# Optimization experiments

Measured on AMD Instinct MI355X. Metric: run time of the kernel, lower is better.

## Reference

```python
import jax, jax.numpy as jnp
import numpy as np

S, B, C = 56, 32, 1024
T = 48
H = 1024          # hidden_size_decoder (== context_size C)
EMB = 512
RANK = 128
VOCAB = 32000


def setup_inputs() -> dict:
    key = jax.random.key(0)
    ks = jax.random.split(key, 16)
    w = 0.05
    inp = {
        "encoded": jax.random.normal(ks[0], (S, B, C), jnp.float32),
        "encoder_state": jax.random.normal(ks[1], (2, B, H), jnp.float32) * 0.1,
        "tgt_tokens": jax.random.randint(ks[2], (B, T), 0, VOCAB),
        "enc_lens": jax.random.randint(ks[3], (B,), S // 2, S + 1).astype(jnp.int32),
        "tgt_lens": jax.random.randint(ks[4], (B,), T // 2, T + 1).astype(jnp.int32),
        "E": jax.random.normal(ks[5], (VOCAB, RANK), jnp.float32) * w,
        "P": jax.random.normal(ks[6], (RANK, EMB), jnp.float32) * w,
        "W0": jax.random.normal(ks[7], (EMB + C, 4 * H), jnp.float32) * w,
        "U0": jax.random.normal(ks[8], (H, 4 * H), jnp.float32) * w,
        "b0": jnp.zeros((4 * H,), jnp.float32),
        "W1": jax.random.normal(ks[9], (H, 4 * H), jnp.float32) * w,
        "U1": jax.random.normal(ks[10], (H, 4 * H), jnp.float32) * w,
        "b1": jnp.zeros((4 * H,), jnp.float32),
        "Wo": jax.random.normal(ks[11], (H + C, EMB), jnp.float32) * w,
        "bo": jnp.zeros((EMB,), jnp.float32),
    }
    return inp


def _lstm_cell(x, h, c, W, U, b):
    gates = x @ W + h @ U + b                      # [B, 4H]
    i, f, g, o = jnp.split(gates, 4, axis=-1)      # torch LSTMCell gate order
    c_new = jax.nn.sigmoid(f) * c + jax.nn.sigmoid(i) * jnp.tanh(g)
    h_new = jax.nn.sigmoid(o) * jnp.tanh(c_new)
    return h_new, c_new


def reference(encoded, encoder_state, tgt_tokens, enc_lens, tgt_lens,
              E, P, W0, U0, b0, W1, U1, b1, Wo, bo):
    # encoded: [S, B, C] (padded encoder outputs), encoder_state: [L=2, B, H]
    enc_b = jnp.transpose(encoded, (1, 0, 2))                 # [B, S, C]
    enc_mask = jnp.arange(S)[None, :] >= enc_lens[:, None]    # [B, S] True = pad

    # factorized embedding lookup (dropout p=0)
    emb = (E[tgt_tokens] @ P)                                 # [B, T, EMB]
    emb_t = jnp.transpose(emb, (1, 0, 2))[: T - 1]            # [T-1, B, EMB]

    h0 = encoder_state                                        # [2, B, H]
    c0 = jnp.zeros_like(encoder_state)
    ctx0 = jnp.zeros((B, C), encoded.dtype)

    def step(carry, x_emb):
        h, c, ctx = carry
        x = jnp.concatenate([x_emb, ctx], axis=-1)            # [B, EMB+C]
        h0n, c0n = _lstm_cell(x, h[0], c[0], W0, U0, b0)
        h1n, c1n = _lstm_cell(h0n, h[1], c[1], W1, U1, b1)
        query = h1n                                           # no context projection
        scores = jnp.einsum("bsc,bc->bs", enc_b, query)       # [B, S]
        scores = jnp.where(enc_mask, -jnp.inf, scores)
        p_att = jax.nn.softmax(scores, axis=-1)
        ctx_new = jnp.einsum("bs,bsc->bc", p_att, enc_b)      # [B, C]
        return (jnp.stack([h0n, h1n]), jnp.stack([c0n, c1n]), ctx_new), (h1n, ctx_new)

    _, (decs, ctxs) = jax.lax.scan(step, (h0, c0, ctx0), emb_t)  # each [T-1, B, *]

    feats = jnp.concatenate([decs, ctxs], axis=-1)            # [T-1, B, H+C]
    hproj = jnp.tanh(feats @ Wo + bo)                          # [T-1, B, EMB]
    logits = (hproj @ P.T) @ E.T                               # [T-1, B, VOCAB]

    labels = tgt_tokens[:, 1:].T                               # [T-1, B]
    logp = jax.nn.log_softmax(logits, axis=-1)
    nll = -jnp.take_along_axis(logp, labels[..., None], axis=-1)[..., 0]
    valid = jnp.arange(T - 1)[:, None] < (tgt_lens[None, :] - 1)  # step t predicts token t+1
    loss = jnp.sum(jnp.where(valid, nll, 0.0))                 # CrossEntropyLoss(reduction='sum')
    return loss
```

## Files before the change

kernel.cpp:

```cpp
#include <hip/hip_runtime.h>
#include <math.h>

#define S_   56
#define B_   32
#define C_   1024
#define T_   48
#define TS   47
#define H_   1024
#define EMB_ 512
#define RANK_ 128
#define VOCAB_ 32000
#define G4   4096
#define NBLK 256

#define FL_DONE 8192
#define FL_P    8224
#define FL_PD   9248
#define FL_SIZE 10240

using bf16x8 = __attribute__((ext_vector_type(8))) __bf16;
using f32x4  = __attribute__((ext_vector_type(4))) float;

__device__ __forceinline__ float sigmoidf_(float x){ return 1.0f/(1.0f+expf(-x)); }
__device__ __forceinline__ float b2f(__bf16 x){ return (float)x; }
__device__ __forceinline__ f32x4 z4(){ f32x4 z = {0.f,0.f,0.f,0.f}; return z; }

#define AG __HIP_MEMORY_SCOPE_AGENT
__device__ __forceinline__ void stc_u64(void* p, unsigned long long v){
  __hip_atomic_store((unsigned long long*)p, v, __ATOMIC_RELAXED, AG);
}
__device__ __forceinline__ void stc_bf16(__bf16* p, __bf16 v){
  union { __bf16 b; unsigned short s; } t; t.b = v;
  __hip_atomic_store((unsigned short*)p, t.s, __ATOMIC_RELAXED, AG);
}

struct RedShared {
  float red[4][2][16][18];
};
struct AttnShared {
  union { float hS[1024]; float cred[3][128][8]; } u;
  float sS[64];
  float pS[64];
};
union alignas(16) SharedU { RedShared r; AttnShared a; };

__device__ __forceinline__ void bar_arrive(unsigned* bars, int bi, unsigned e){
  asm volatile("s_waitcnt vmcnt(0)" ::: "memory");
  __syncthreads();
  if (threadIdx.x == 0)
    __hip_atomic_store(bars + (size_t)bi*32, e, __ATOMIC_RELAXED, AG);
}
__device__ __forceinline__ void bar_wait(unsigned* bars, int bi, unsigned e){
  if (bi == 0){
    if (threadIdx.x < 256){
      while (__hip_atomic_load(bars + (size_t)threadIdx.x*32, __ATOMIC_RELAXED, AG) < e)
        __builtin_amdgcn_s_sleep(1);
    }
    __syncthreads();
    if (threadIdx.x == 0)
      __hip_atomic_store(bars + FL_DONE, e, __ATOMIC_RELAXED, AG);
  } else {
    if (threadIdx.x == 0){
      while (__hip_atomic_load(bars + FL_DONE, __ATOMIC_RELAXED, AG) < e)
        __builtin_amdgcn_s_sleep(1);
    }
    __syncthreads();
  }
  asm volatile("" ::: "memory");
}
__device__ __forceinline__ void pflag_wait(unsigned* bars, int bi, unsigned t){
  if (bi == 0){
    if (threadIdx.x < 32){
      while (__hip_atomic_load(bars + FL_P + (size_t)threadIdx.x*32, __ATOMIC_RELAXED, AG) < t)
        __builtin_amdgcn_s_sleep(1);
    }
    __syncthreads();
    if (threadIdx.x == 0)
      __hip_atomic_store(bars + FL_PD, t, __ATOMIC_RELAXED, AG);
  } else {
    if (threadIdx.x == 0){
      while (__hip_atomic_load(bars + FL_PD, __ATOMIC_RELAXED, AG) < t)
        __builtin_amdgcn_s_sleep(1);
    }
    __syncthreads();
  }
  asm volatile("" ::: "memory");
}

__global__ void k_init(const float* __restrict__ es, __bf16* h0bm1, __bf16* fm1,
                       unsigned* bars){
  int i = blockIdx.x*blockDim.x + threadIdx.x;
  if (i < 32*H_){
    int b = i >> 10, j = i & 1023;
    h0bm1[(size_t)b*1024 + j]       = (__bf16)es[i];
    fm1[(size_t)b*2048 + j]         = (__bf16)es[32*H_ + i];
    fm1[(size_t)b*2048 + 1024 + j]  = (__bf16)0.0f;
  }
  if (i < FL_SIZE) bars[i] = 0u;
}

__global__ void k_cvt(const float* __restrict__ src, __bf16* __restrict__ dst, int n){
  int i = (blockIdx.x*blockDim.x + threadIdx.x)*4;
  if (i < n){
    float4 v = *(const float4*)(src + i);
    dst[i+0]=(__bf16)v.x; dst[i+1]=(__bf16)v.y; dst[i+2]=(__bf16)v.z; dst[i+3]=(__bf16)v.w;
  }
}

__global__ void k_embed(const float* __restrict__ E, const float* __restrict__ P,
                        const int* __restrict__ tok, __bf16* __restrict__ embb){
  int blk = blockIdx.x;
  int t = blk >> 5, b = blk & 31, tid = threadIdx.x;
  __shared__ float er[RANK_];
  int tk = tok[b*T_ + t];
  er[tid] = E[(size_t)tk*RANK_ + tid];
  __syncthreads();
  float4 acc = {0.f,0.f,0.f,0.f};
  int e = tid*4;
  for (int r2 = 0; r2 < RANK_; r2++){
    float ev = er[r2];
    float4 p = *(const float4*)(P + (size_t)r2*EMB_ + e);
    acc.x += ev*p.x; acc.y += ev*p.y; acc.z += ev*p.z; acc.w += ev*p.w;
  }
  size_t o = (size_t)blk*EMB_ + e;
  embb[o+0]=(__bf16)acc.x; embb[o+1]=(__bf16)acc.y;
  embb[o+2]=(__bf16)acc.z; embb[o+3]=(__bf16)acc.w;
}

__global__ void k_pack2(const float* __restrict__ W, int K1, const float* __restrict__ U,
                        __bf16* __restrict__ dst, int NCH){
  int ch = blockIdx.x;
  int g  = blockIdx.y >> 2;
  int band = blockIdx.y & 3;
  int tid = threadIdx.x;
  __shared__ __bf16 Tl[32][264];
  {
    int r = tid>>3, cs = tid&7;
    int kk = ch*32 + r;
    const float* src = (kk < K1) ? (W + (size_t)kk*G4 + g*1024 + band*256 + cs*32)
                                 : (U + (size_t)(kk-K1)*G4 + g*1024 + band*256 + cs*32);
    #pragma unroll
    for (int u=0;u<8;u++){
      float4 v = *(const float4*)(src + u*4);
      Tl[r][cs*32+u*4+0]=(__bf16)v.x; Tl[r][cs*32+u*4+1]=(__bf16)v.y;
      Tl[r][cs*32+u*4+2]=(__bf16)v.z; Tl[r][cs*32+u*4+3]=(__bf16)v.w;
    }
  }
  __syncthreads();
  int bil = tid>>2, aq = tid&3;
  int bi = band*64 + bil;
  #pragma unroll
  for (int q=0;q<4;q++){
    __bf16 o8[8];
    #pragma unroll
    for (int i=0;i<8;i++) o8[i] = Tl[aq*8+i][bil*4+q];
    int lane = aq*16 + g*4 + q;
    *(bf16x8*)(dst + (((size_t)bi*NCH + ch)*64 + lane)*8) = *(bf16x8*)o8;
  }
}

__global__ void k_packB(const float* __restrict__ src, __bf16* __restrict__ dst,
                        int K, int N, int tr){
  int kk0 = blockIdx.x*32, j0 = blockIdx.y*16, lane = threadIdx.x;
  int am = lane&15, aq = lane>>4;
  int j = j0 + am;
  __bf16 o8[8];
  #pragma unroll
  for (int i=0;i<8;i++){
    int k = kk0 + aq*8 + i;
    float v = tr ? src[(size_t)j*K + k] : src[(size_t)k*N + j];
    o8[i] = (__bf16)v;
  }
  int NCH = K/32, jt = j0>>4, ch = kk0>>5;
  *(bf16x8*)(dst + (((size_t)jt*NCH + ch)*64 + lane)*8) = *(bf16x8*)o8;
}

template<int NC>
__device__ __forceinline__ void accum(f32x4& acc0, f32x4& acc1,
    const __bf16* __restrict__ abase, int rs, const __bf16* wlds,
    int ch0, int am, int aq, int lane)
{
  const __bf16* a0p = abase + (size_t)am*rs + aq*8;
  const __bf16* a1p = abase + (size_t)(am+16)*rs + aq*8;
  const __bf16* wl  = wlds + (size_t)lane*8;
  #pragma unroll
  for (int c=0;c<NC;c++){
    int ch = ch0 + c;
    bf16x8 a0 = *(const bf16x8*)(a0p + (size_t)ch*32);
    bf16x8 a1 = *(const bf16x8*)(a1p + (size_t)ch*32);
    bf16x8 w  = *(const bf16x8*)(wl  + (size_t)ch*512);
    acc0 = __builtin_amdgcn_mfma_f32_16x16x32_bf16(a0, w, acc0, 0, 0, 0);
    acc1 = __builtin_amdgcn_mfma_f32_16x16x32_bf16(a1, w, acc1, 0, 0, 0);
  }
}

__device__ __forceinline__ void reduce_cell(SharedU& su, const f32x4& acc0, const f32x4& acc1,
    int bi, int tid, const float* __restrict__ bias, float& creg,
    __bf16* __restrict__ hout, int stride)
{
  int kw = tid>>6, lane = tid&63, am = lane&15, aq = lane>>4;
  if (kw >= 4){
    #pragma unroll
    for (int rg=0;rg<4;rg++){
      su.r.red[kw-4][0][aq*4+rg][am] = acc0[rg];
      su.r.red[kw-4][1][aq*4+rg][am] = acc1[rg];
    }
  }
  __syncthreads();
  if (kw < 4){
    #pragma unroll
    for (int rg=0;rg<4;rg++){
      su.r.red[kw][0][aq*4+rg][am] += acc0[rg];
      su.r.red[kw][1][aq*4+rg][am] += acc1[rg];
    }
  }
  __syncthreads();
  if (tid < 128){
    int b = tid>>2, q = tid&3;
    int mt = b>>4, r = b&15;
    float G0=0.f, G1=0.f, G2=0.f, G3=0.f;
    #pragma unroll
    for (int w2=0; w2<4; w2++){
      G0 += su.r.red[w2][mt][r][q];
      G1 += su.r.red[w2][mt][r][4+q];
      G2 += su.r.red[w2][mt][r][8+q];
      G3 += su.r.red[w2][mt][r][12+q];
    }
    int j = bi*4 + q;
    float gi = G0 + bias[j];
    float gf = G1 + bias[1024 + j];
    float gg = G2 + bias[2048 + j];
    float go = G3 + bias[3072 + j];
    float ii = sigmoidf_(gi), ff = sigmoidf_(gf), gv = tanhf(gg), oo = sigmoidf_(go);
    float cv = ff*creg + ii*gv;
    float hv = oo*tanhf(cv);
    creg = cv;
    stc_bf16(hout + (size_t)b*stride + j, (__bf16)hv);
  }
}

__device__ __forceinline__ void attn_block(AttnShared& sa, int b, int tid,
    const __bf16* __restrict__ encb, const int* __restrict__ enc_lens,
    __bf16* __restrict__ fbt)
{
  if (tid < 128){
    bf16x8 h8 = *(const bf16x8*)(fbt + (size_t)b*2048 + tid*8);
    #pragma unroll
    for (int u=0;u<8;u++) sa.u.hS[tid*8+u] = b2f(h8[u]);
  }
  __syncthreads();
  int w = tid >> 6, lane = tid & 63;
  for (int s = w; s < S_; s += 8){
    const __bf16* er = encb + ((size_t)s*32 + b)*C_;
    float a = 0.f;
    #pragma unroll
    for (int half = 0; half < 2; half++){
      int k = lane*8 + half*512;
      bf16x8 e8 = *(const bf16x8*)(er + k);
      #pragma unroll
      for (int u=0;u<8;u++) a += b2f(e8[u]) * sa.u.hS[k+u];
    }
    #pragma unroll
    for (int off=32; off>0; off>>=1) a += __shfl_down(a, off);
    if (lane == 0) sa.sS[s] = a;
  }
  __syncthreads();
  if (tid < 64){
    int len = enc_lens[b];
    float sc = (tid < len && tid < S_) ? sa.sS[tid] : -1e30f;
    float m = sc;
    #pragma unroll
    for (int off=32; off>0; off>>=1) m = fmaxf(m, __shfl_xor(m, off));
    float e = expf(sc - m);
    float ssum = e;
    #pragma unroll
    for (int off=32; off>0; off>>=1) ssum += __shfl_xor(ssum, off);
    sa.pS[tid] = e / ssum;
  }
  __syncthreads();
  int cg = tid & 127, sg = tid >> 7;
  float a8[8];
  #pragma unroll
  for (int i=0;i<8;i++) a8[i] = 0.f;
  for (int s = sg; s < S_; s += 4){
    float p = sa.pS[s];
    bf16x8 e8 = *(const bf16x8*)(encb + ((size_t)s*32 + b)*C_ + cg*8);
    #pragma unroll
    for (int i=0;i<8;i++) a8[i] += p * b2f(e8[i]);
  }
  if (sg > 0){
    #pragma unroll
    for (int i=0;i<8;i++) sa.u.cred[sg-1][cg][i] = a8[i];
  }
  __syncthreads();
  if (sg == 0){
    union { __bf16 bb[8]; unsigned long long u[2]; } cu;
    #pragma unroll
    for (int i=0;i<8;i++){
      float v = a8[i] + sa.u.cred[0][cg][i] + sa.u.cred[1][cg][i] + sa.u.cred[2][cg][i];
      cu.bb[i] = (__bf16)v;
    }
    stc_u64(fbt + (size_t)b*2048 + 1024 + cg*8,     cu.u[0]);
    stc_u64(fbt + (size_t)b*2048 + 1024 + cg*8 + 4, cu.u[1]);
  }
}

__global__ __launch_bounds__(512) void k_loop(
    const __bf16* __restrict__ WP0, const __bf16* __restrict__ WP1,
    const float* __restrict__ b0, const float* __restrict__ b1,
    __bf16* __restrict__ h0b,
    __bf16* __restrict__ featsb,
    const __bf16* __restrict__ embb,
    const __bf16* __restrict__ encb, const int* __restrict__ enc_lens,
    unsigned* bars)
{
  __shared__ __bf16 wB0[80*512];
  __shared__ __bf16 wB1[64*512];
  __shared__ SharedU su;
  int bi = blockIdx.x, tid = threadIdx.x;
  int kw = tid>>6, lane = tid&63, am = lane&15, aq = lane>>4;

  {
    const bf16x8* g0 = (const bf16x8*)(WP0 + (size_t)bi*80*512);
    const bf16x8* g1 = (const bf16x8*)(WP1 + (size_t)bi*64*512);
    bf16x8* l0 = (bf16x8*)wB0;
    bf16x8* l1 = (bf16x8*)wB1;
    for (int idx = tid; idx < 80*64; idx += 512) l0[idx] = g0[idx];
    for (int idx = tid; idx < 64*64; idx += 512) l1[idx] = g1[idx];
  }
  __syncthreads();

  float c0r = 0.f, c1r = 0.f;
  f32x4 g00 = z4(), g01 = z4(), g10 = z4(), g11 = z4();

  accum<2>(g00, g01, embb,                 512,  wB0, kw*2,    am, aq, lane);
  accum<4>(g00, g01, h0b - 32768 - 1536,   1024, wB0, 48+kw*4, am, aq, lane);

  unsigned e = 0;
  for (int t = 0; t < TS; t++){
    const __bf16* fprev = featsb + ((size_t)(t-1))*65536;
    __bf16* h0t = h0b + (size_t)t*32768;
    __bf16* ft  = featsb + (size_t)t*65536;

    pflag_wait(bars, bi, (unsigned)t);
    accum<4>(g00, g01, fprev + 512, 2048, wB0, 16+kw*4, am, aq, lane);
    reduce_cell(su, g00, g01, bi, tid, b0, c0r, h0t, 1024);
    g00 = z4(); g01 = z4();
    bar_arrive(bars, bi, ++e);
    accum<4>(g10, g11, fprev - 1024, 2048, wB1, 32+kw*4, am, aq, lane);
    bar_wait(bars, bi, e);

    accum<4>(g10, g11, h0t, 1024, wB1, kw*4, am, aq, lane);
    reduce_cell(su, g10, g11, bi, tid, b1, c1r, ft, 2048);
    g10 = z4(); g11 = z4();
    bar_arrive(bars, bi, ++e);
    if (t + 1 < TS){
      accum<2>(g00, g01, embb + (size_t)(t+1)*16384, 512,  wB0, kw*2,    am, aq, lane);
      accum<4>(g00, g01, h0t - 1536,                 1024, wB0, 48+kw*4, am, aq, lane);
    }
    bar_wait(bars, bi, e);

    if (bi < 32){
      attn_block(su.a, bi, tid, encb, enc_lens, ft);
      asm volatile("s_waitcnt vmcnt(0)" ::: "memory");
      __syncthreads();
      if (tid == 0)
        __hip_atomic_store(bars + FL_P + (size_t)bi*32, (unsigned)(t+1), __ATOMIC_RELAXED, AG);
    }
  }
}

__global__ __launch_bounds__(256) void k_hproj_mfma(
    const __bf16* __restrict__ fb, const __bf16* __restrict__ WoP,
    const float* __restrict__ bo, __bf16* __restrict__ hpb)
{
  int nt = blockIdx.x, jb = blockIdx.y, tid = threadIdx.x;
  int w = tid>>6, lane = tid&63;
  int mt = w&1, jw = w>>1;
  int am = lane&15, aq = lane>>4;
  const __bf16* aRow = fb + ((size_t)(nt*32 + mt*16 + am))*2048 + aq*8;
  int jt = jb*2 + jw;
  const __bf16* bptr = WoP + ((size_t)jt*64)*512 + lane*8;
  f32x4 acc = {0,0,0,0};
  bf16x8 ar0 = *(const bf16x8*)(aRow);
  bf16x8 br0 = *(const bf16x8*)(bptr);
  bf16x8 ar1 = *(const bf16x8*)(aRow + 32);
  bf16x8 br1 = *(const bf16x8*)(bptr + 512);
  for (int ch = 0; ch < 64; ch += 2){
    bf16x8 a0 = ar0, b0 = br0, a1 = ar1, b1 = br1;
    if (ch + 2 < 64){
      ar0 = *(const bf16x8*)(aRow + (ch+2)*32);
      br0 = *(const bf16x8*)(bptr + (size_t)(ch+2)*512);
      ar1 = *(const bf16x8*)(aRow + (ch+3)*32);
      br1 = *(const bf16x8*)(bptr + (size_t)(ch+3)*512);
    }
    acc = __builtin_amdgcn_mfma_f32_16x16x32_bf16(a0, b0, acc, 0, 0, 0);
    acc = __builtin_amdgcn_mfma_f32_16x16x32_bf16(a1, b1, acc, 0, 0, 0);
  }
  int jcol = jb*32 + jw*16 + am;
  float bv = bo[jcol];
  #pragma unroll
  for (int rg=0; rg<4; rg++){
    int m = nt*32 + mt*16 + aq*4 + rg;
    hpb[(size_t)m*512 + jcol] = (__bf16)tanhf(acc[rg] + bv);
  }
}

__global__ __launch_bounds__(256) void k_rproj_mfma(
    const __bf16* __restrict__ hpb, const __bf16* __restrict__ PP,
    __bf16* __restrict__ rb)
{
  int nt = blockIdx.x, jb = blockIdx.y, tid = threadIdx.x;
  int w = tid>>6, lane = tid&63;
  int mt = w&1, jw = w>>1;
  int am = lane&15, aq = lane>>4;
  const __bf16* aRow = hpb + ((size_t)(nt*32 + mt*16 + am))*512 + aq*8;
  int jt = jb*2 + jw;
  const __bf16* bptr = PP + ((size_t)jt*16)*512 + lane*8;
  f32x4 acc = {0,0,0,0};
  #pragma unroll
  for (int ch = 0; ch < 16; ch++){
    bf16x8 a = *(const bf16x8*)(aRow + ch*32);
    bf16x8 b = *(const bf16x8*)(bptr + (size_t)ch*512);
    acc = __builtin_amdgcn_mfma_f32_16x16x32_bf16(a, b, acc, 0, 0, 0);
  }
  int jcol = jb*32 + jw*16 + am;
  #pragma unroll
  for (int rg=0; rg<4; rg++){
    int m = nt*32 + mt*16 + aq*4 + rg;
    rb[(size_t)m*RANK_ + jcol] = (__bf16)acc[rg];
  }
}

__global__ __launch_bounds__(256) void k_vocab2(
    const __bf16* __restrict__ rb, const __bf16* __restrict__ Eb,
    const int* __restrict__ tok,
    float* __restrict__ mpart, float* __restrict__ lpart,
    float* __restrict__ lablog)
{
  int vc = blockIdx.x, tid = threadIdx.x;
  int w = tid>>6, lane = tid&63;
  int am = lane&15, aq = lane>>4;
  int vb = vc*128 + w*32;
  bf16x8 bfr[2][4];
  #pragma unroll
  for (int vt=0; vt<2; vt++)
    #pragma unroll
    for (int ks=0; ks<4; ks++)
      bfr[vt][ks] = *(const bf16x8*)(Eb + ((size_t)(vb + vt*16 + am))*RANK_ + ks*32 + aq*8);

  __shared__ float redM[4][32], redL[4][32];
  for (int nt = 0; nt < TS; nt++){
    f32x4 acc[2][2] = {{{0,0,0,0},{0,0,0,0}},{{0,0,0,0},{0,0,0,0}}};
    #pragma unroll
    for (int mt=0; mt<2; mt++){
      #pragma unroll
      for (int ks=0; ks<4; ks++){
        bf16x8 a = *(const bf16x8*)(rb + ((size_t)(nt*32 + mt*16 + am))*RANK_ + ks*32 + aq*8);
        acc[mt][0] = __builtin_amdgcn_mfma_f32_16x16x32_bf16(a, bfr[0][ks], acc[mt][0], 0,0,0);
        acc[mt][1] = __builtin_amdgcn_mfma_f32_16x16x32_bf16(a, bfr[1][ks], acc[mt][1], 0,0,0);
      }
    }
    #pragma unroll
    for (int mt=0; mt<2; mt++){
      #pragma unroll
      for (int rg=0; rg<4; rg++){
        int row = mt*16 + aq*4 + rg;
        int n = nt*32 + row;
        int lbl = tok[row*T_ + nt + 1];
        float v0 = acc[mt][0][rg], v1 = acc[mt][1][rg];
        if (vb + am == lbl)      lablog[n] = v0;
        if (vb + 16 + am == lbl) lablog[n] = v1;
        float m = fmaxf(v0, v1);
        #pragma unroll
        for (int off=1; off<16; off<<=1) m = fmaxf(m, __shfl_xor(m, off));
        float l = expf(v0 - m) + expf(v1 - m);
        #pragma unroll
        for (int off=1; off<16; off<<=1) l += __shfl_xor(l, off);
        if (am == 0){ redM[w][row] = m; redL[w][row] = l; }
      }
    }
    __syncthreads();
    if (tid < 32){
      float M = fmaxf(fmaxf(redM[0][tid], redM[1][tid]), fmaxf(redM[2][tid], redM[3][tid]));
      float L = 0.f;
      #pragma unroll
      for (int ww=0; ww<4; ww++) L += redL[ww][tid]*expf(redM[ww][tid] - M);
      mpart[(size_t)(nt*32 + tid)*250 + vc] = M;
      lpart[(size_t)(nt*32 + tid)*250 + vc] = L;
    }
    __syncthreads();
  }
}

__global__ void k_loss1(const float* __restrict__ mpart, const float* __restrict__ lpart,
                        const float* __restrict__ lablog, const int* __restrict__ tgt_lens,
                        float* __restrict__ tpart){
  int t = blockIdx.x, tid = threadIdx.x;
  int row = tid >> 3, cq = tid & 7;
  int n = t*32 + row;
  float m = -1e30f;
  for (int c = cq; c < 250; c += 8) m = fmaxf(m, mpart[(size_t)n*250 + c]);
  #pragma unroll
  for (int off=1; off<8; off<<=1) m = fmaxf(m, __shfl_xor(m, off));
  float l = 0.f;
  for (int c = cq; c < 250; c += 8) l += lpart[(size_t)n*250 + c]*expf(mpart[(size_t)n*250 + c] - m);
  #pragma unroll
  for (int off=1; off<8; off<<=1) l += __shfl_xor(l, off);
  __shared__ float red[32];
  if (cq == 0)
    red[row] = (t < tgt_lens[row] - 1) ? (m + logf(l) - lablog[n]) : 0.f;
  __syncthreads();
  if (tid == 0){
    float s = 0.f;
    #pragma unroll
    for (int i=0;i<32;i++) s += red[i];
    tpart[t] = s;
  }
}

__global__ void k_loss2(const float* __restrict__ tpart, float* __restrict__ out){
  int tid = threadIdx.x;
  float v = (tid < TS) ? tpart[tid] : 0.f;
  #pragma unroll
  for (int off=32; off>0; off>>=1) v += __shfl_down(v, off);
  if (tid == 0) out[0] = v;
}

extern "C" void kernel_launch(void* const* d_in, const int* in_sizes, int n_in,
                              void* d_out, int out_size, void* d_ws, size_t ws_size,
                              hipStream_t stream){
  const float* enc      = (const float*)d_in[0];
  const float* es       = (const float*)d_in[1];
  const int*   tok      = (const int*)  d_in[2];
  const int*   enc_lens = (const int*)  d_in[3];
  const int*   tgt_lens = (const int*)  d_in[4];
  const float* E        = (const float*)d_in[5];
  const float* P        = (const float*)d_in[6];
  const float* W0       = (const float*)d_in[7];
  const float* U0       = (const float*)d_in[8];
  const float* b0       = (const float*)d_in[9];
  const float* W1       = (const float*)d_in[10];
  const float* U1       = (const float*)d_in[11];
  const float* b1       = (const float*)d_in[12];
  const float* Wo       = (const float*)d_in[13];
  const float* bo       = (const float*)d_in[14];
  float* out = (float*)d_out;

  float* fb = (float*)d_ws;
  size_t fo = 0;
  float* mpart = fb + fo; fo += (size_t)TS*32*250;
  float* lpart = fb + fo; fo += (size_t)TS*32*250;
  float* lab   = fb + fo; fo += (size_t)TS*32;
  float* tpart = fb + fo; fo += 64;
  unsigned* bars = (unsigned*)(fb + fo); fo += FL_SIZE;
  __bf16* bb = (__bf16*)(fb + fo);
  size_t bo2 = 0;
  __bf16* WP0    = bb + bo2; bo2 += (size_t)4096*2560;
  __bf16* WP1    = bb + bo2; bo2 += (size_t)4096*2048;
  __bf16* encb   = bb + bo2; bo2 += (size_t)S_*32*C_;
  __bf16* embb   = bb + bo2; bo2 += (size_t)TS*32*EMB_;
  __bf16* rbuf   = bb + bo2; bo2 += (size_t)TS*32*RANK_;
  __bf16* WoP    = bb + bo2; bo2 += (size_t)2048*512;
  __bf16* PP     = bb + bo2; bo2 += (size_t)512*128;
  __bf16* featsb0= bb + bo2; bo2 += (size_t)(TS+1)*32*2048;
  __bf16* hpb    = bb + bo2; bo2 += (size_t)TS*32*EMB_;
  __bf16* h0b0   = bb + bo2; bo2 += (size_t)(TS+1)*32*1024;
  __bf16* Eb     = WP0;

  __bf16* featsb = featsb0 + (size_t)32*2048;
  __bf16* h0b    = h0b0 + (size_t)32*1024;

  k_init<<<128, 256, 0, stream>>>(es, h0b0, featsb0, bars);
  k_cvt<<<(S_*32*C_/4 + 255)/256, 256, 0, stream>>>(enc, encb, S_*32*C_);
  k_embed<<<TS*32, 128, 0, stream>>>(E, P, tok, embb);
  k_pack2<<<dim3(80,16), 256, 0, stream>>>(W0, 1536, U0, WP0, 80);
  k_pack2<<<dim3(64,16), 256, 0, stream>>>(W1, 1024, U1, WP1, 64);
  k_packB<<<dim3(64,32), 64, 0, stream>>>(Wo, WoP, 2048, 512, 0);
  k_packB<<<dim3(16,8), 64, 0, stream>>>(P, PP, 512, 128, 1);

  k_loop<<<NBLK, 512, 0, stream>>>(WP0, WP1, b0, b1, h0b, featsb,
                                   embb, encb, enc_lens, bars);

  k_cvt<<<(VOCAB_*RANK_/4 + 255)/256, 256, 0, stream>>>(E, Eb, VOCAB_*RANK_);

  k_hproj_mfma<<<dim3(TS,16), 256, 0, stream>>>(featsb, WoP, bo, hpb);
  k_rproj_mfma<<<dim3(TS,4), 256, 0, stream>>>(hpb, PP, rbuf);
  k_vocab2<<<250, 256, 0, stream>>>(rbuf, Eb, tok, mpart, lpart, lab);
  k_loss1<<<TS, 256, 0, stream>>>(mpart, lpart, lab, tgt_lens, tpart);
  k_loss2<<<1, 64, 0, stream>>>(tpart, out);
}
```

Measured before the change: 1.426 ms.

## Split attention across 64 blocks, restructure grid barriers, pack hidden-state stores

Attention for each batch row now runs on two blocks, each computing half of the context columns, with 8 reduction groups instead of 4. Only the 64 attention blocks wait on the second barrier, and they poll all arrival flags directly instead of waiting for a leader block to publish a done flag. Non-attention blocks go straight to the next step's pflag wait. The pflag wait now has every block poll the 64 producer flags directly, removing the leader-block relay. The other spin loops drop their sleep. The four per-gate bf16 hidden-state stores are packed into one 64-bit store via lane shuffles. The aim is shorter serial latency per timestep, at the cost of more global polling traffic and duplicated score computation across the two attention halves.

Result: faster. 1.392 ms (-2.4%).

```diff
diff --git a/kernel.cpp b/kernel.cpp
--- a/kernel.cpp
+++ b/kernel.cpp
@@ -15,8 +15,7 @@
 
 #define FL_DONE 8192
 #define FL_P    8224
-#define FL_PD   9248
-#define FL_SIZE 10240
+#define FL_SIZE 10496
 
 using bf16x8 = __attribute__((ext_vector_type(8))) __bf16;
 using f32x4  = __attribute__((ext_vector_type(4))) float;
@@ -28,17 +27,13 @@
 #define AG __HIP_MEMORY_SCOPE_AGENT
 __device__ __forceinline__ void stc_u64(void* p, unsigned long long v){
   __hip_atomic_store((unsigned long long*)p, v, __ATOMIC_RELAXED, AG);
-}
-__device__ __forceinline__ void stc_bf16(__bf16* p, __bf16 v){
-  union { __bf16 b; unsigned short s; } t; t.b = v;
-  __hip_atomic_store((unsigned short*)p, t.s, __ATOMIC_RELAXED, AG);
 }
 
 struct RedShared {
   float red[4][2][16][18];
 };
 struct AttnShared {
-  union { float hS[1024]; float cred[3][128][8]; } u;
+  union { float hS[1024]; float cred[7][64][8]; } u;
   float sS[64];
   float pS[64];
 };
@@ -50,40 +45,35 @@
   if (threadIdx.x == 0)
     __hip_atomic_store(bars + (size_t)bi*32, e, __ATOMIC_RELAXED, AG);
 }
-__device__ __forceinline__ void bar_wait(unsigned* bars, int bi, unsigned e){
-  if (bi == 0){
+__device__ __forceinline__ void bar_wait_all(unsigned* bars, int bi, unsigned e){
+  if (bi == 255){
     if (threadIdx.x < 256){
-      while (__hip_atomic_load(bars + (size_t)threadIdx.x*32, __ATOMIC_RELAXED, AG) < e)
-        __builtin_amdgcn_s_sleep(1);
+      while (__hip_atomic_load(bars + (size_t)threadIdx.x*32, __ATOMIC_RELAXED, AG) < e) {}
     }
     __syncthreads();
     if (threadIdx.x == 0)
       __hip_atomic_store(bars + FL_DONE, e, __ATOMIC_RELAXED, AG);
   } else {
     if (threadIdx.x == 0){
-      while (__hip_atomic_load(bars + FL_DONE, __ATOMIC_RELAXED, AG) < e)
-        __builtin_amdgcn_s_sleep(1);
+      while (__hip_atomic_load(bars + FL_DONE, __ATOMIC_RELAXED, AG) < e) {}
     }
     __syncthreads();
   }
   asm volatile("" ::: "memory");
 }
-__device__ __forceinline__ void pflag_wait(unsigned* bars, int bi, unsigned t){
-  if (bi == 0){
-    if (threadIdx.x < 32){
-      while (__hip_atomic_load(bars + FL_P + (size_t)threadIdx.x*32, __ATOMIC_RELAXED, AG) < t)
-        __builtin_amdgcn_s_sleep(1);
-    }
-    __syncthreads();
-    if (threadIdx.x == 0)
-      __hip_atomic_store(bars + FL_PD, t, __ATOMIC_RELAXED, AG);
-  } else {
-    if (threadIdx.x == 0){
-      while (__hip_atomic_load(bars + FL_PD, __ATOMIC_RELAXED, AG) < t)
-        __builtin_amdgcn_s_sleep(1);
-    }
-    __syncthreads();
-  }
+__device__ __forceinline__ void bar_wait_direct(unsigned* bars, unsigned e){
+  if (threadIdx.x < 256){
+    while (__hip_atomic_load(bars + (size_t)threadIdx.x*32, __ATOMIC_RELAXED, AG) < e) {}
+  }
+  __syncthreads();
+  asm volatile("" ::: "memory");
+}
+__device__ __forceinline__ void pflag_wait(unsigned* bars, unsigned t){
+  if (threadIdx.x < 64){
+    while (__hip_atomic_load(bars + FL_P + (size_t)threadIdx.x*32, __ATOMIC_RELAXED, AG) < t)
+      __builtin_amdgcn_s_sleep(2);
+  }
+  __syncthreads();
   asm volatile("" ::: "memory");
 }
 
@@ -235,11 +225,22 @@
     float cv = ff*creg + ii*gv;
     float hv = oo*tanhf(cv);
     creg = cv;
-    stc_bf16(hout + (size_t)b*stride + j, (__bf16)hv);
-  }
-}
-
-__device__ __forceinline__ void attn_block(AttnShared& sa, int b, int tid,
+    union { __bf16 h; unsigned short s; } hu; hu.h = (__bf16)hv;
+    unsigned h0v = hu.s;
+    unsigned h1v = __shfl_down(h0v, 1);
+    unsigned h2v = __shfl_down(h0v, 2);
+    unsigned h3v = __shfl_down(h0v, 3);
+    if (q == 0){
+      unsigned long long pk = (unsigned long long)(h0v & 0xffffu)
+                            | ((unsigned long long)(h1v & 0xffffu) << 16)
+                            | ((unsigned long long)(h2v & 0xffffu) << 32)
+                            | ((unsigned long long)(h3v & 0xffffu) << 48);
+      stc_u64(hout + (size_t)b*stride + bi*4, pk);
+    }
+  }
+}
+
+__device__ __forceinline__ void attn_block(AttnShared& sa, int b, int chalf, int tid,
     const __bf16* __restrict__ encb, const int* __restrict__ enc_lens,
     __bf16* __restrict__ fbt)
 {
@@ -278,13 +279,13 @@
     sa.pS[tid] = e / ssum;
   }
   __syncthreads();
-  int cg = tid & 127, sg = tid >> 7;
+  int cg = tid & 63, sg = tid >> 6;
   float a8[8];
   #pragma unroll
   for (int i=0;i<8;i++) a8[i] = 0.f;
-  for (int s = sg; s < S_; s += 4){
+  for (int s = sg; s < S_; s += 8){
     float p = sa.pS[s];
-    bf16x8 e8 = *(const bf16x8*)(encb + ((size_t)s*32 + b)*C_ + cg*8);
+    bf16x8 e8 = *(const bf16x8*)(encb + ((size_t)s*32 + b)*C_ + chalf*512 + cg*8);
     #pragma unroll
     for (int i=0;i<8;i++) a8[i] += p * b2f(e8[i]);
   }
@@ -297,11 +298,13 @@
     union { __bf16 bb[8]; unsigned long long u[2]; } cu;
     #pragma unroll
     for (int i=0;i<8;i++){
-      float v = a8[i] + sa.u.cred[0][cg][i] + sa.u.cred[1][cg][i] + sa.u.cred[2][cg][i];
+      float v = a8[i];
+      #pragma unroll
+      for (int k=0;k<7;k++) v += sa.u.cred[k][cg][i];
       cu.bb[i] = (__bf16)v;
     }
-    stc_u64(fbt + (size_t)b*2048 + 1024 + cg*8,     cu.u[0]);
-    stc_u64(fbt + (size_t)b*2048 + 1024 + cg*8 + 4, cu.u[1]);
+    stc_u64(fbt + (size_t)b*2048 + 1024 + chalf*512 + cg*8,     cu.u[0]);
+    stc_u64(fbt + (size_t)b*2048 + 1024 + chalf*512 + cg*8 + 4, cu.u[1]);
   }
 }
 
@@ -342,13 +345,13 @@
     __bf16* h0t = h0b + (size_t)t*32768;
     __bf16* ft  = featsb + (size_t)t*65536;
 
-    pflag_wait(bars, bi, (unsigned)t);
+    pflag_wait(bars, (unsigned)t);
     accum<4>(g00, g01, fprev + 512, 2048, wB0, 16+kw*4, am, aq, lane);
     reduce_cell(su, g00, g01, bi, tid, b0, c0r, h0t, 1024);
     g00 = z4(); g01 = z4();
     bar_arrive(bars, bi, ++e);
     accum<4>(g10, g11, fprev - 1024, 2048, wB1, 32+kw*4, am, aq, lane);
-    bar_wait(bars, bi, e);
+    bar_wait_all(bars, bi, e);
 
     accum<4>(g10, g11, h0t, 1024, wB1, kw*4, am, aq, lane);
     reduce_cell(su, g10, g11, bi, tid, b1, c1r, ft, 2048);
@@ -358,10 +361,10 @@
       accum<2>(g00, g01, embb + (size_t)(t+1)*16384, 512,  wB0, kw*2,    am, aq, lane);
       accum<4>(g00, g01, h0t - 1536,                 1024, wB0, 48+kw*4, am, aq, lane);
     }
-    bar_wait(bars, bi, e);
-
-    if (bi < 32){
-      attn_block(su.a, bi, tid, encb, enc_lens, ft);
+
+    if (bi < 64){
+      bar_wait_direct(bars, e);
+      attn_block(su.a, bi & 31, bi >> 5, tid, encb, enc_lens, ft);
       asm volatile("s_waitcnt vmcnt(0)" ::: "memory");
       __syncthreads();
       if (tid == 0)
```
